# Optimization experiments

Measured on AMD Instinct MI355X. Metric: run time of the kernel, lower is better.

## Reference

```python
import jax, jax.numpy as jnp
import numpy as np
import math

ROPE_BASE = 10000.0
ALIBI_SLOPE = 2.0 ** (-8.0)  # _get_alibi_slopes(1) == [2**(-8*1/1)]


def _rope_cos_sin(T, d):
    inv_freq = 1.0 / (ROPE_BASE ** (jnp.arange(0, d, 2, dtype=jnp.float32) / d))
    t = jnp.arange(T, dtype=jnp.float32)
    freqs = jnp.einsum('i,j->ij', t, inv_freq)          # [T, d/2]
    emb = jnp.concatenate([freqs, freqs], axis=-1)      # [T, d]
    return jnp.cos(emb), jnp.sin(emb)


def _rotate_half(x):
    x1, x2 = jnp.split(x, 2, axis=-1)
    return jnp.concatenate([-x2, x1], axis=-1)


def setup_inputs() -> dict:
    key = jax.random.key(0)
    kq, kk, kv = jax.random.split(key, 3)
    B, T, H = 8, 2048, 256
    return {
        'q': jax.random.normal(kq, (B, T, H), dtype=jnp.float32),
        'k': jax.random.normal(kk, (B, T, H), dtype=jnp.float32),
        'v': jax.random.normal(kv, (B, T, H), dtype=jnp.float32),
    }


def reference(q, k, v):
    B, T, H = q.shape  # num_heads == 1, so head_dim == H
    cos, sin = _rope_cos_sin(T, H)                      # [T, H]
    qe = q * cos + _rotate_half(q) * sin                # [B, T, H]
    ke = k * cos + _rotate_half(k) * sin                # [B, T, H]

    scale = 1.0 / math.sqrt(H)
    scores = jnp.einsum('btd,bsd->bts', qe, ke) * scale  # [B, T, T]

    pos = jnp.arange(T)
    rel = (pos[None, :] - pos[:, None]).astype(jnp.float32)  # [T, T]
    alibi = (ALIBI_SLOPE * rel)[None, None, :, :]            # [1, 1, T, T]

    # torch broadcast: [B,T,T] + [1,1,T,T] -> [1,B,T,T]
    scores = scores + alibi
    attn = jax.nn.softmax(scores, axis=-1)              # [1, B, T, T]
    out = jnp.matmul(attn, v)                           # [1, B, T, H]
    return out
```

## Files before the change

kernel.cpp:

```cpp
#include <hip/hip_runtime.h>

#define B_ 8
#define T_ 2048
#define H_ 256
#define PSTR 72
#define SCALE2 0.0901684403f
#define SLOPE2 0.00563552752f
#define ELEMS ((size_t)B_ * T_ * H_)

typedef __attribute__((ext_vector_type(8))) short bf16x8;
typedef __attribute__((ext_vector_type(4))) float f32x4;

#define MFMA16(a, b, c) __builtin_amdgcn_mfma_f32_16x16x32_bf16((a), (b), (c), 0, 0, 0)

__device__ __forceinline__ ushort f2bf(float f) {
  unsigned u = __float_as_uint(f);
  u += 0x7FFFu + ((u >> 16) & 1u);
  return (ushort)(u >> 16);
}

__device__ __forceinline__ void gl_lds16(const ushort* g, ushort* l) {
  __builtin_amdgcn_global_load_lds(
      (const __attribute__((address_space(1))) unsigned int*)g,
      (__attribute__((address_space(3))) unsigned int*)l, 16, 0, 0);
}

__global__ void prep_kernel(const float* __restrict__ k, const float* __restrict__ v,
                            ushort* __restrict__ kt, ushort* __restrict__ vt) {
  __shared__ ushort tile[64][72];
  const int bid = blockIdx.x;
  const int tid = threadIdx.x;
  if (bid < 1024) {
    int idx = bid * 256 + tid;
    int d8 = idx & 15;
    int bt = idx >> 4;
    int t = bt & (T_ - 1);
    int b = bt >> 11;
    size_t base = (size_t)bt * H_ + d8 * 8;
    float4 a0 = *(const float4*)(k + base);
    float4 a1 = *(const float4*)(k + base + 4);
    float4 c0 = *(const float4*)(k + base + 128);
    float4 c1 = *(const float4*)(k + base + 132);
    float av[8] = {a0.x, a0.y, a0.z, a0.w, a1.x, a1.y, a1.z, a1.w};
    float cv[8] = {c0.x, c0.y, c0.z, c0.w, c1.x, c1.y, c1.z, c1.w};
    bf16x8 lo, hi;
#pragma unroll
    for (int e = 0; e < 8; ++e) {
      int j = d8 * 8 + e;
      float rv = (float)t * exp2f((float)j * -0.103810252959f) * 0.15915494309f;
      float fr = rv - floorf(rv);
      float sn = __builtin_amdgcn_sinf(fr), cs = __builtin_amdgcn_cosf(fr);
      lo[e] = (short)f2bf(av[e] * cs - cv[e] * sn);
      hi[e] = (short)f2bf(cv[e] * cs + av[e] * sn);
    }
    size_t kdst = (((size_t)(b * 64 + (t >> 5)) * 32 + d8) * 32 + (t & 31)) * 8;
    *(bf16x8*)(kt + kdst) = lo;
    *(bf16x8*)(kt + kdst + 4096) = hi;
  } else {
    int bid2 = bid - 1024;
    int b = bid2 >> 7, rem = bid2 & 127;
    int h0 = (rem >> 5) * 64, t0 = (rem & 31) * 64;
    int c4 = tid & 15, r0 = tid >> 4;
#pragma unroll
    for (int p = 0; p < 4; ++p) {
      int row = r0 + p * 16;
      const float4 f = *(const float4*)(v + ((size_t)(b * T_ + t0 + row)) * H_ + h0 + c4 * 4);
      ushort4 u;
      u.x = f2bf(f.x); u.y = f2bf(f.y); u.z = f2bf(f.z); u.w = f2bf(f.w);
      *(ushort4*)&tile[row][(c4 * 4) ^ (8 * ((row >> 3) & 7))] = u;
    }
    __syncthreads();
#pragma unroll
    for (int p = 0; p < 2; ++p) {
      int c = tid + p * 256;
      int h = c >> 3, tc = (c & 7) * 8;
      int xo = 8 * (c & 7);
      ushort4 u0, u1;
      u0.x = tile[tc + 0][h ^ xo]; u0.y = tile[tc + 1][h ^ xo];
      u0.z = tile[tc + 2][h ^ xo]; u0.w = tile[tc + 3][h ^ xo];
      u1.x = tile[tc + 4][h ^ xo]; u1.y = tile[tc + 5][h ^ xo];
      u1.z = tile[tc + 6][h ^ xo]; u1.w = tile[tc + 7][h ^ xo];
      int tg = t0 + tc;
      size_t dst = (((size_t)(b * 64 + (tg >> 5)) * 4 + ((tg >> 3) & 3)) * 256 + (h0 + h)) * 8;
      *(ushort4*)(vt + dst) = u0;
      *(ushort4*)(vt + dst + 4) = u1;
    }
  }
}

__global__ __launch_bounds__(512, 2)
void attn_kernel(const float* __restrict__ q, const ushort* __restrict__ kt,
                 const ushort* __restrict__ vt, float* __restrict__ out,
                 float* __restrict__ o1, float* __restrict__ lpart) {
  __shared__ ushort Ksh[2][16384];
  __shared__ ushort Vsh[2][16384];
  __shared__ ushort Psh[8][16 * PSTR];

  const int tid = threadIdx.x;
  const int w = tid >> 6, lane = tid & 63, quad = lane >> 4, l16 = lane & 15;
  const int b = blockIdx.x;
  const int q0 = blockIdx.y * 128;
  const int sp = blockIdx.z;
  const int kvb = sp * (T_ / 2);
  const int niter = 16;

  bf16x8 aq[8];
  {
    const float* qb = q + ((size_t)(b * T_) + q0 + w * 16) * H_;
    const int t = q0 + w * 16 + l16;
    float qv[8][8];
#pragma unroll
    for (int ks = 0; ks < 8; ++ks) {
      float4 x0 = *(const float4*)(qb + (size_t)l16 * H_ + ks * 32 + quad * 8);
      float4 x1 = *(const float4*)(qb + (size_t)l16 * H_ + ks * 32 + quad * 8 + 4);
      qv[ks][0] = x0.x; qv[ks][1] = x0.y; qv[ks][2] = x0.z; qv[ks][3] = x0.w;
      qv[ks][4] = x1.x; qv[ks][5] = x1.y; qv[ks][6] = x1.z; qv[ks][7] = x1.w;
    }
#pragma unroll
    for (int ks = 0; ks < 4; ++ks)
#pragma unroll
      for (int e = 0; e < 8; ++e) {
        int d = ks * 32 + quad * 8 + e;
        float rv = (float)t * exp2f((float)d * -0.103810252959f) * 0.15915494309f;
        float fr = rv - floorf(rv);
        float sn = __builtin_amdgcn_sinf(fr), cs = __builtin_amdgcn_cosf(fr);
        aq[ks][e]     = (short)f2bf(qv[ks][e] * cs - qv[ks + 4][e] * sn);
        aq[ks + 4][e] = (short)f2bf(qv[ks + 4][e] * cs + qv[ks][e] * sn);
      }
  }

  const f32x4 fzero = {0.f, 0.f, 0.f, 0.f};
  f32x4 O[16], lac = fzero;
#pragma unroll
  for (int ht = 0; ht < 16; ++ht) O[ht] = fzero;
  bf16x8 vones;
#pragma unroll
  for (int i = 0; i < 8; ++i) vones[i] = (short)0x3F80;

  const ushort* ktb = kt + (size_t)(b * 64 + sp * 32) * 8192;
  const ushort* vtb = vt + (size_t)(b * 64 + sp * 32) * 8192;
  const int stoff = tid * 8;

#pragma unroll
  for (int i = 0; i < 4; ++i)
    gl_lds16(ktb + stoff + i * 4096, &Ksh[0][stoff + i * 4096]);
  __builtin_amdgcn_sched_barrier(0);
#pragma unroll
  for (int i = 0; i < 4; ++i)
    gl_lds16(ktb + 16384 + stoff + i * 4096, &Ksh[1][stoff + i * 4096]);
  __builtin_amdgcn_sched_barrier(0);
#pragma unroll
  for (int i = 0; i < 4; ++i)
    gl_lds16(vtb + stoff + i * 4096, &Vsh[0][stoff + i * 4096]);

  const float arb = SLOPE2 * (float)(q0 + w * 16 + quad * 4);
  f32x4 s_prev[4] = {fzero, fzero, fzero, fzero};

  {
    __builtin_amdgcn_sched_barrier(0);
    __builtin_amdgcn_s_waitcnt(0x0F78);
    __builtin_amdgcn_s_barrier();
    __builtin_amdgcn_sched_barrier(0);
#pragma unroll
    for (int ks = 0; ks < 8; ++ks)
#pragma unroll
      for (int nt = 0; nt < 4; ++nt) {
        bf16x8 kf = *(const bf16x8*)&Ksh[0][(nt >> 1) * 8192 +
            ((ks * 4 + quad) * 32 + (nt & 1) * 16 + l16) * 8];
        s_prev[nt] = MFMA16(aq[ks], kf, s_prev[nt]);
      }
    __builtin_amdgcn_sched_barrier(0);
    __builtin_amdgcn_s_waitcnt(0xC07F);
    __builtin_amdgcn_s_barrier();
    __builtin_amdgcn_sched_barrier(0);
#pragma unroll
    for (int i = 0; i < 4; ++i)
      gl_lds16(ktb + (size_t)2 * 16384 + stoff + i * 4096, &Ksh[0][stoff + i * 4096]);
    __builtin_amdgcn_sched_barrier(0);
#pragma unroll
    for (int i = 0; i < 4; ++i)
      gl_lds16(vtb + (size_t)1 * 16384 + stoff + i * 4096, &Vsh[1][stoff + i * 4096]);
  }

  for (int it = 1; it < niter; ++it) {
    const int p = it & 1;
    __builtin_amdgcn_sched_barrier(0);
    if (it == niter - 1) __builtin_amdgcn_s_waitcnt(0x0F74);
    else                 __builtin_amdgcn_s_waitcnt(0x0F78);
    __builtin_amdgcn_s_barrier();
    __builtin_amdgcn_sched_barrier(0);

    f32x4 s_cur[4] = {fzero, fzero, fzero, fzero};
#pragma unroll
    for (int ks = 0; ks < 8; ++ks)
#pragma unroll
      for (int nt = 0; nt < 4; ++nt) {
        bf16x8 kf = *(const bf16x8*)&Ksh[p][(nt >> 1) * 8192 +
            ((ks * 4 + quad) * 32 + (nt & 1) * 16 + l16) * 8];
        s_cur[nt] = MFMA16(aq[ks], kf, s_cur[nt]);
      }

#pragma unroll
    for (int nt = 0; nt < 4; ++nt) {
      float ac = SLOPE2 * (float)(kvb + (it - 1) * 64 + nt * 16 + l16);
#pragma unroll
      for (int r = 0; r < 4; ++r) {
        float a0 = ac - arb - SLOPE2 * (float)r;
        float pv = __builtin_amdgcn_exp2f(fmaf(s_prev[nt][r], SCALE2, a0));
        Psh[w][(quad * 4 + r) * PSTR + nt * 16 + l16] = f2bf(pv);
      }
    }

    bf16x8 pf0 = *(const bf16x8*)&Psh[w][l16 * PSTR + quad * 8];
    bf16x8 pf1 = *(const bf16x8*)&Psh[w][l16 * PSTR + 32 + quad * 8];
    lac = MFMA16(pf0, vones, lac);
    lac = MFMA16(pf1, vones, lac);
#pragma unroll
    for (int ht = 0; ht < 16; ++ht) {
      bf16x8 vf0 = *(const bf16x8*)&Vsh[1 - p][(quad * 256 + ht * 16 + l16) * 8];
      bf16x8 vf1 = *(const bf16x8*)&Vsh[1 - p][8192 + (quad * 256 + ht * 16 + l16) * 8];
      O[ht] = MFMA16(pf0, vf0, O[ht]);
      O[ht] = MFMA16(pf1, vf1, O[ht]);
    }

#pragma unroll
    for (int nt = 0; nt < 4; ++nt) s_prev[nt] = s_cur[nt];

    __builtin_amdgcn_sched_barrier(0);
    __builtin_amdgcn_s_waitcnt(0xC07F);
    __builtin_amdgcn_s_barrier();
    __builtin_amdgcn_sched_barrier(0);

    if (it < niter - 2) {
      const ushort* kg = ktb + (size_t)(it + 2) * 16384;
#pragma unroll
      for (int i = 0; i < 4; ++i)
        gl_lds16(kg + stoff + i * 4096, &Ksh[p][stoff + i * 4096]);
    }
    __builtin_amdgcn_sched_barrier(0);
    if (it < niter - 1) {
      const ushort* vg = vtb + (size_t)(it + 1) * 16384;
#pragma unroll
      for (int i = 0; i < 4; ++i)
        gl_lds16(vg + stoff + i * 4096, &Vsh[1 - p][stoff + i * 4096]);
    }
  }

  {
    __builtin_amdgcn_sched_barrier(0);
    __builtin_amdgcn_s_waitcnt(0x0070);
    __builtin_amdgcn_s_barrier();
    __builtin_amdgcn_sched_barrier(0);
#pragma unroll
    for (int nt = 0; nt < 4; ++nt) {
      float ac = SLOPE2 * (float)(kvb + (niter - 1) * 64 + nt * 16 + l16);
#pragma unroll
      for (int r = 0; r < 4; ++r) {
        float a0 = ac - arb - SLOPE2 * (float)r;
        float pv = __builtin_amdgcn_exp2f(fmaf(s_prev[nt][r], SCALE2, a0));
        Psh[w][(quad * 4 + r) * PSTR + nt * 16 + l16] = f2bf(pv);
      }
    }
    bf16x8 pf0 = *(const bf16x8*)&Psh[w][l16 * PSTR + quad * 8];
    bf16x8 pf1 = *(const bf16x8*)&Psh[w][l16 * PSTR + 32 + quad * 8];
    lac = MFMA16(pf0, vones, lac);
    lac = MFMA16(pf1, vones, lac);
#pragma unroll
    for (int ht = 0; ht < 16; ++ht) {
      bf16x8 vf0 = *(const bf16x8*)&Vsh[1][(quad * 256 + ht * 16 + l16) * 8];
      bf16x8 vf1 = *(const bf16x8*)&Vsh[1][8192 + (quad * 256 + ht * 16 + l16) * 8];
      O[ht] = MFMA16(pf0, vf0, O[ht]);
      O[ht] = MFMA16(pf1, vf1, O[ht]);
    }
  }

  float* od = (sp == 0) ? out : o1;
  float* ob = od + ((size_t)(b * T_) + q0 + w * 16) * H_;
#pragma unroll
  for (int r = 0; r < 4; ++r) {
    int row = quad * 4 + r;
#pragma unroll
    for (int ht = 0; ht < 16; ++ht)
      ob[(size_t)row * H_ + ht * 16 + l16] = O[ht][r];
  }
  if (l16 == 0) {
#pragma unroll
    for (int r = 0; r < 4; ++r)
      lpart[(size_t)(sp * B_ + b) * T_ + q0 + w * 16 + quad * 4 + r] = lac[r];
  }
}

__global__ void combine_kernel(float* __restrict__ out, const float* __restrict__ o1,
                               const float* __restrict__ lpart) {
  int idx = blockIdx.x * 256 + threadIdx.x;
  int row = idx >> 6;
  float inv = 1.0f / (lpart[row] + lpart[B_ * T_ + row]);
  float4 a = ((const float4*)out)[idx];
  float4 c = ((const float4*)o1)[idx];
  a.x = (a.x + c.x) * inv; a.y = (a.y + c.y) * inv;
  a.z = (a.z + c.z) * inv; a.w = (a.w + c.w) * inv;
  ((float4*)out)[idx] = a;
}

extern "C" void kernel_launch(void* const* d_in, const int* in_sizes, int n_in,
                              void* d_out, int out_size, void* d_ws, size_t ws_size,
                              hipStream_t stream) {
  const float* q = (const float*)d_in[0];
  const float* k = (const float*)d_in[1];
  const float* v = (const float*)d_in[2];
  float* out = (float*)d_out;

  ushort* kt = (ushort*)d_ws;
  ushort* vt = kt + ELEMS;
  float* o1 = (float*)(vt + ELEMS);
  float* lpart = o1 + ELEMS;

  prep_kernel<<<dim3(2048), 256, 0, stream>>>(k, v, kt, vt);
  attn_kernel<<<dim3(B_, T_ / 128, 2), 512, 0, stream>>>(q, kt, vt, out, o1, lpart);
  combine_kernel<<<dim3((B_ * T_ * H_ / 4) / 256), 256, 0, stream>>>(out, o1, lpart);
}
```

Measured before the change: 144.9 us.

## Fuse split-KV combine into attention kernel via atomic ticket last-block reduction

```diff
diff --git a/kernel.cpp b/kernel.cpp
--- a/kernel.cpp
+++ b/kernel.cpp
@@ -26,10 +26,12 @@
 }
 
 __global__ void prep_kernel(const float* __restrict__ k, const float* __restrict__ v,
-                            ushort* __restrict__ kt, ushort* __restrict__ vt) {
+                            ushort* __restrict__ kt, ushort* __restrict__ vt,
+                            unsigned* __restrict__ tickets) {
   __shared__ ushort tile[64][72];
   const int bid = blockIdx.x;
   const int tid = threadIdx.x;
+  if (bid == 0 && tid < B_ * 16) tickets[tid] = 0u;
   if (bid < 1024) {
     int idx = bid * 256 + tid;
     int d8 = idx & 15;
@@ -91,10 +93,12 @@
 __global__ __launch_bounds__(512, 2)
 void attn_kernel(const float* __restrict__ q, const ushort* __restrict__ kt,
                  const ushort* __restrict__ vt, float* __restrict__ out,
-                 float* __restrict__ o1, float* __restrict__ lpart) {
+                 float* __restrict__ opart, float* __restrict__ lpart,
+                 unsigned* __restrict__ tickets) {
   __shared__ ushort Ksh[2][16384];
   __shared__ ushort Vsh[2][16384];
   __shared__ ushort Psh[8][16 * PSTR];
+  __shared__ unsigned tkt_s;
 
   const int tid = threadIdx.x;
   const int w = tid >> 6, lane = tid & 63, quad = lane >> 4, l16 = lane & 15;
@@ -274,32 +278,41 @@
     }
   }
 
-  float* od = (sp == 0) ? out : o1;
-  float* ob = od + ((size_t)(b * T_) + q0 + w * 16) * H_;
-#pragma unroll
-  for (int r = 0; r < 4; ++r) {
-    int row = quad * 4 + r;
-#pragma unroll
-    for (int ht = 0; ht < 16; ++ht)
-      ob[(size_t)row * H_ + ht * 16 + l16] = O[ht][r];
-  }
-  if (l16 == 0) {
-#pragma unroll
-    for (int r = 0; r < 4; ++r)
-      lpart[(size_t)(sp * B_ + b) * T_ + q0 + w * 16 + quad * 4 + r] = lac[r];
-  }
-}
-
-__global__ void combine_kernel(float* __restrict__ out, const float* __restrict__ o1,
-                               const float* __restrict__ lpart) {
-  int idx = blockIdx.x * 256 + threadIdx.x;
-  int row = idx >> 6;
-  float inv = 1.0f / (lpart[row] + lpart[B_ * T_ + row]);
-  float4 a = ((const float4*)out)[idx];
-  float4 c = ((const float4*)o1)[idx];
-  a.x = (a.x + c.x) * inv; a.y = (a.y + c.y) * inv;
-  a.z = (a.z + c.z) * inv; a.w = (a.w + c.w) * inv;
-  ((float4*)out)[idx] = a;
+  {
+    float* ob = opart + (size_t)sp * ELEMS + ((size_t)(b * T_) + q0 + w * 16) * H_;
+#pragma unroll
+    for (int r = 0; r < 4; ++r) {
+      int row = quad * 4 + r;
+#pragma unroll
+      for (int ht = 0; ht < 16; ++ht)
+        ob[(size_t)row * H_ + ht * 16 + l16] = O[ht][r];
+    }
+    if (l16 == 0) {
+#pragma unroll
+      for (int r = 0; r < 4; ++r)
+        lpart[(size_t)(sp * B_ + b) * T_ + q0 + w * 16 + quad * 4 + r] = lac[r];
+    }
+  }
+  __threadfence();
+  __syncthreads();
+  if (tid == 0) tkt_s = atomicAdd(&tickets[b * 16 + blockIdx.y], 1u);
+  __syncthreads();
+  if (tkt_s == 1) {
+    __threadfence();
+    const int osp = 1 - sp;
+    const float* pb = opart + (size_t)osp * ELEMS + ((size_t)(b * T_) + q0 + w * 16) * H_;
+    float* ob = out + ((size_t)(b * T_) + q0 + w * 16) * H_;
+#pragma unroll
+    for (int r = 0; r < 4; ++r) {
+      int row = quad * 4 + r;
+      float lo = lpart[(size_t)(osp * B_ + b) * T_ + q0 + w * 16 + row];
+      float inv = 1.0f / (lac[r] + lo);
+#pragma unroll
+      for (int ht = 0; ht < 16; ++ht)
+        ob[(size_t)row * H_ + ht * 16 + l16] =
+            (O[ht][r] + pb[(size_t)row * H_ + ht * 16 + l16]) * inv;
+    }
+  }
 }
 
 extern "C" void kernel_launch(void* const* d_in, const int* in_sizes, int n_in,
@@ -312,10 +325,11 @@
 
   ushort* kt = (ushort*)d_ws;
   ushort* vt = kt + ELEMS;
-  float* o1 = (float*)(vt + ELEMS);
-  float* lpart = o1 + ELEMS;
-
-  prep_kernel<<<dim3(2048), 256, 0, stream>>>(k, v, kt, vt);
-  attn_kernel<<<dim3(B_, T_ / 128, 2), 512, 0, stream>>>(q, kt, vt, out, o1, lpart);
-  combine_kernel<<<dim3((B_ * T_ * H_ / 4) / 256), 256, 0, stream>>>(out, o1, lpart);
-}
+  float* opart = (float*)(vt + ELEMS);
+  float* lpart = opart + 2 * ELEMS;
+  unsigned* tickets = (unsigned*)(lpart + (size_t)2 * B_ * T_);
+
+  prep_kernel<<<dim3(2048), 256, 0, stream>>>(k, v, kt, vt, tickets);
+  attn_kernel<<<dim3(B_, T_ / 128, 2), 512, 0, stream>>>(q, kt, vt, out, opart,
+                                                         lpart, tickets);
+}
```

After: 229.8 us. 1.59x slower.
